# Kernel optimization log

Hardware: AMD Instinct MI355X
Metric: run time of the kernel (lower is better)

## Reference

```python
import jax, jax.numpy as jnp
import numpy as np

B, IN, EMB, HID, HYP, NZ = 8192, 512, 512, 1024, 256, 64
EPS = 1e-5


def _ln(x, g, b):
    # layernorm over last axis; g/b broadcast
    m = x.mean(-1, keepdims=True)
    v = x.var(-1, keepdims=True)
    return (x - m) * jax.lax.rsqrt(v + EPS) * g + b


def setup_inputs() -> dict:
    key = jax.random.key(0)
    ks = jax.random.split(key, 16)
    s = lambda i, shape: jax.random.normal(ks[i], shape, jnp.float32) * 0.02
    return dict(
        x=jax.random.normal(ks[0], (B, IN), jnp.float32),
        e=jax.random.normal(ks[1], (B, EMB), jnp.float32),
        h=jax.random.normal(ks[2], (B, HID), jnp.float32),
        c=jax.random.normal(ks[3], (B, HID), jnp.float32),
        h_hat=jax.random.normal(ks[4], (B, HYP), jnp.float32),
        c_hat=jax.random.normal(ks[5], (B, HYP), jnp.float32),
        # inner layer-normed LSTMCell(embedding_size, hyper_size) params
        hyper_Wx=s(6, (4 * HYP, EMB)),
        hyper_Wh=s(7, (4 * HYP, HYP)),
        hyper_b=jnp.zeros((4 * HYP,), jnp.float32),
        hyper_ln_g=jnp.ones((4, HYP), jnp.float32),
        hyper_ln_b=jnp.zeros((4, HYP), jnp.float32),
        hyper_lnc_g=jnp.ones((HYP,), jnp.float32),
        hyper_lnc_b=jnp.zeros((HYP,), jnp.float32),
        # z projections (hyper -> 4*n_z)
        zh_W=s(8, (4 * NZ, HYP)), zh_b=jnp.zeros((4 * NZ,), jnp.float32),
        zx_W=s(9, (4 * NZ, HYP)), zx_b=jnp.zeros((4 * NZ,), jnp.float32),
        zb_W=s(10, (4 * NZ, HYP)),
        # per-gate d projections (n_z -> hidden), no bias
        dh_W=s(11, (4, HID, NZ)),
        dx_W=s(12, (4, HID, NZ)),
        # outer LSTM weight matrices (zeros in torch init; randn here so outputs are nontrivial)
        w_h=s(13, (4, HID, HID)),
        w_x=s(14, (4, HID, IN)),
    )


def reference(x, e, h, c, h_hat, c_hat,
              hyper_Wx, hyper_Wh, hyper_b, hyper_ln_g, hyper_ln_b,
              hyper_lnc_g, hyper_lnc_b,
              zh_W, zh_b, zx_W, zx_b, zb_W, dh_W, dx_W, w_h, w_x):
    # --- inner layer-normed hyper LSTM cell ---
    ifgo = e @ hyper_Wx.T + h_hat @ hyper_Wh.T + hyper_b            # [B, 4*HYP]
    ifgo = _ln(ifgo.reshape(B, 4, HYP), hyper_ln_g, hyper_ln_b)     # per-gate LN
    i_g, f_g, g_g, o_g = (ifgo[:, k] for k in range(4))
    c_hat_n = jax.nn.sigmoid(f_g) * c_hat + jax.nn.sigmoid(i_g) * jnp.tanh(g_g)
    h_hat_n = jax.nn.sigmoid(o_g) * jnp.tanh(_ln(c_hat_n, hyper_lnc_g, hyper_lnc_b))
    # --- z vectors, chunked into 4 gates along last dim ---
    z_h = (h_hat_n @ zh_W.T + zh_b).reshape(B, 4, NZ)
    z_x = (h_hat_n @ zx_W.T + zx_b).reshape(B, 4, NZ)
    z_b = (h_hat_n @ zb_W.T).reshape(B, 4, NZ)
    # --- per-gate weight modulation: d = Linear(z); dhw = d @ W ---
    d_h = jnp.einsum('bgz,ghz->gbh', z_h, dh_W)        # [4, B, HID]
    d_x = jnp.einsum('bgz,ghz->gbh', z_x, dx_W)        # [4, B, HID]
    dhw_h = jnp.einsum('gbh,ghk->gbk', d_h, w_h)       # [4, B, HID]
    dhw_x = jnp.einsum('gbh,ghk->gbk', d_x, w_x)       # [4, B, IN]
    return dhw_h, dhw_x, jnp.transpose(z_b, (1, 0, 2))  # z_b chunks as [4, B, NZ]
```

## Files before the change

### kernel.cpp

```cpp
#include <hip/hip_runtime.h>
#include <cstddef>

constexpr int Bn   = 8192;
constexpr int INn  = 512;
constexpr int EMBn = 512;
constexpr int HIDn = 1024;
constexpr int HYPn = 256;
constexpr int NZn  = 64;
constexpr float EPS = 1e-5f;

typedef unsigned short u16;
typedef unsigned int   u32;
typedef float f32x4 __attribute__((ext_vector_type(4)));
typedef short s16x8 __attribute__((ext_vector_type(8)));

__device__ __forceinline__ u16 f2bf(float x) {
    u32 u = __float_as_uint(x);
    u = (u + 0x7FFFu + ((u >> 16) & 1u)) >> 16;
    return (u16)u;
}
__device__ __forceinline__ float bf2f(u16 h) {
    return __uint_as_float(((u32)h) << 16);
}

__global__ __launch_bounds__(256) void k_prep(
    const float* __restrict__ e,  const float* __restrict__ hh,
    const float* __restrict__ wx, const float* __restrict__ wh,
    u16* __restrict__ eHi, u16* __restrict__ eLo,
    u16* __restrict__ hhHi, u16* __restrict__ hhLo,
    u16* __restrict__ wxHi, u16* __restrict__ wxLo,
    u16* __restrict__ whHi, u16* __restrict__ whLo)
{
    long u = (long)blockIdx.x * 256 + threadIdx.x;
    const long U_E  = (long)Bn * EMBn / 8;
    const long U_H  = (long)Bn * HYPn / 8;
    const long U_WX = (long)HIDn * EMBn / 8;
    const float* src; u16 *hi, *lo; int ld, kblks;
    if (u < U_E)                    { src = e;  hi = eHi;  lo = eLo;  ld = EMBn; kblks = EMBn / 32; }
    else if (u < U_E + U_H)         { u -= U_E; src = hh; hi = hhHi; lo = hhLo; ld = HYPn; kblks = HYPn / 32; }
    else if (u < U_E + U_H + U_WX)  { u -= U_E + U_H; src = wx; hi = wxHi; lo = wxLo; ld = EMBn; kblks = EMBn / 32; }
    else                            { u -= U_E + U_H + U_WX; src = wh; hi = whHi; lo = whLo; ld = HYPn; kblks = HYPn / 32; }

    const long lu = u;
    const long perBlk = (long)kblks * 512;
    const int blk  = (int)(u / perBlk);
    const int rem  = (int)(u % perBlk);
    const int kblk = rem >> 9;
    const int r2   = rem & 511;
    const int grp  = r2 >> 6;
    const int lane = r2 & 63;
    const int row  = blk * 128 + grp * 16 + (lane & 15);
    const int k    = kblk * 32 + (lane >> 4) * 8;

    const float4 v0 = *(const float4*)(src + (size_t)row * ld + k);
    const float4 v1 = *(const float4*)(src + (size_t)row * ld + k + 4);
    const float f[8] = {v0.x, v0.y, v0.z, v0.w, v1.x, v1.y, v1.z, v1.w};
    union { u16 us[8]; uint4 v; } H, L;
#pragma unroll
    for (int j = 0; j < 8; ++j) {
        const u16 h = f2bf(f[j]);
        H.us[j] = h;
        L.us[j] = f2bf(f[j] - bf2f(h));
    }
    *(uint4*)(hi + lu * 8) = H.v;
    *(uint4*)(lo + lu * 8) = L.v;
}

__global__ __launch_bounds__(256) void k_ifgo_mfma(
    const u16* __restrict__ eHi,  const u16* __restrict__ eLo,
    const u16* __restrict__ hhHi, const u16* __restrict__ hhLo,
    const u16* __restrict__ wxHi, const u16* __restrict__ wxLo,
    const u16* __restrict__ whHi, const u16* __restrict__ whLo,
    const float* __restrict__ bias, float* __restrict__ ifgo)
{
    __shared__ __align__(16) u16 lds[4 * 4096];
    const int t = threadIdx.x;
    const int w = t >> 6, l = t & 63;
    const int wr = w >> 1, wc = w & 1;
    const int bx = blockIdx.x, by = blockIdx.y;

    f32x4 acc[4][4] = {};

    for (int s = 0; s < 24; ++s) {
        const bool seg0 = s < 16;
        const u16* aH = seg0 ? eHi  : hhHi;
        const u16* aL = seg0 ? eLo  : hhLo;
        const u16* bH = seg0 ? wxHi : whHi;
        const u16* bL = seg0 ? wxLo : whLo;
        const int kblks = seg0 ? 16 : 8;
        const int kb    = seg0 ? s : s - 16;
        const long ca = ((long)bx * kblks + kb) * 512;
        const long cb = ((long)by * kblks + kb) * 512;

        __syncthreads();
#pragma unroll
        for (int i = 0; i < 2; ++i) {
            const int un = i * 256 + t;
            __builtin_amdgcn_global_load_lds(
                (const __attribute__((address_space(1))) u32*)(aH + (ca + un) * 8),
                (__attribute__((address_space(3))) u32*)(lds + 0 * 4096 + un * 8), 16, 0, 0);
            __builtin_amdgcn_global_load_lds(
                (const __attribute__((address_space(1))) u32*)(aL + (ca + un) * 8),
                (__attribute__((address_space(3))) u32*)(lds + 1 * 4096 + un * 8), 16, 0, 0);
            __builtin_amdgcn_global_load_lds(
                (const __attribute__((address_space(1))) u32*)(bH + (cb + un) * 8),
                (__attribute__((address_space(3))) u32*)(lds + 2 * 4096 + un * 8), 16, 0, 0);
            __builtin_amdgcn_global_load_lds(
                (const __attribute__((address_space(1))) u32*)(bL + (cb + un) * 8),
                (__attribute__((address_space(3))) u32*)(lds + 3 * 4096 + un * 8), 16, 0, 0);
        }
        __syncthreads();

        s16x8 ah[4], al[4], bh[4], bl[4];
#pragma unroll
        for (int f = 0; f < 4; ++f) {
            const int ua = ((wr * 4 + f) * 64 + l) * 8;
            const int ub = ((wc * 4 + f) * 64 + l) * 8;
            ah[f] = *(const s16x8*)(lds + 0 * 4096 + ua);
            al[f] = *(const s16x8*)(lds + 1 * 4096 + ua);
            bh[f] = *(const s16x8*)(lds + 2 * 4096 + ub);
            bl[f] = *(const s16x8*)(lds + 3 * 4096 + ub);
        }
#pragma unroll
        for (int fm = 0; fm < 4; ++fm)
#pragma unroll
            for (int fn = 0; fn < 4; ++fn) {
                acc[fm][fn] = __builtin_amdgcn_mfma_f32_16x16x32_bf16(ah[fm], bh[fn], acc[fm][fn], 0, 0, 0);
                acc[fm][fn] = __builtin_amdgcn_mfma_f32_16x16x32_bf16(ah[fm], bl[fn], acc[fm][fn], 0, 0, 0);
                acc[fm][fn] = __builtin_amdgcn_mfma_f32_16x16x32_bf16(al[fm], bh[fn], acc[fm][fn], 0, 0, 0);
            }
    }

    const int row0 = bx * 128 + wr * 64;
    const int col0 = by * 128 + wc * 64;
    float bv[4];
#pragma unroll
    for (int fn = 0; fn < 4; ++fn) bv[fn] = bias[col0 + fn * 16 + (l & 15)];
#pragma unroll
    for (int fm = 0; fm < 4; ++fm) {
        const int r0 = row0 + fm * 16 + (l >> 4) * 4;
#pragma unroll
        for (int fn = 0; fn < 4; ++fn) {
            const int c = col0 + fn * 16 + (l & 15);
#pragma unroll
            for (int r = 0; r < 4; ++r)
                ifgo[(size_t)(r0 + r) * (4 * HYPn) + c] = acc[fm][fn][r] + bv[fn];
        }
    }
}

__device__ __forceinline__ void nt_accum(
    const float* __restrict__ A, const float* __restrict__ Bm,
    int K, int lda, int ldb, int row0, int col0, int t,
    float acc[4][4], float* As, float* Bs)
{
    const int lr = t >> 2;
    const int lk = (t & 3) << 2;
    const int ty = t >> 4;
    const int tx = t & 15;
    for (int k0 = 0; k0 < K; k0 += 16) {
        const float4 av = *(const float4*)(A  + (size_t)(row0 + lr) * lda + k0 + lk);
        const float4 bv = *(const float4*)(Bm + (size_t)(col0 + lr) * ldb + k0 + lk);
        __syncthreads();
        As[(lk + 0) * 68 + lr] = av.x; As[(lk + 1) * 68 + lr] = av.y;
        As[(lk + 2) * 68 + lr] = av.z; As[(lk + 3) * 68 + lr] = av.w;
        Bs[(lk + 0) * 68 + lr] = bv.x; Bs[(lk + 1) * 68 + lr] = bv.y;
        Bs[(lk + 2) * 68 + lr] = bv.z; Bs[(lk + 3) * 68 + lr] = bv.w;
        __syncthreads();
#pragma unroll
        for (int kk = 0; kk < 16; ++kk) {
            const float4 a = *(const float4*)(As + kk * 68 + ty * 4);
            const float4 b = *(const float4*)(Bs + kk * 68 + tx * 4);
            const float ar[4] = {a.x, a.y, a.z, a.w};
            const float br[4] = {b.x, b.y, b.z, b.w};
#pragma unroll
            for (int i = 0; i < 4; ++i)
#pragma unroll
                for (int j = 0; j < 4; ++j)
                    acc[i][j] = fmaf(ar[i], br[j], acc[i][j]);
        }
    }
}

__global__ __launch_bounds__(256) void k_cell(
    const float* __restrict__ ifgo, const float* __restrict__ c_hat,
    const float* __restrict__ ln_g, const float* __restrict__ ln_b,
    const float* __restrict__ lnc_g, const float* __restrict__ lnc_b,
    float* __restrict__ h_hat_n)
{
    const int row = blockIdx.x;
    const int t = threadIdx.x;
    const int lane = t & 63;
    const int wid = t >> 6;

    __shared__ float act[4][256];
    __shared__ float red[8];

    const float4 v = *(const float4*)(ifgo + (size_t)row * 1024 + t * 4);
    float s  = v.x + v.y + v.z + v.w;
    float ss = v.x * v.x + v.y * v.y + v.z * v.z + v.w * v.w;
#pragma unroll
    for (int off = 32; off > 0; off >>= 1) {
        s  += __shfl_xor(s, off);
        ss += __shfl_xor(ss, off);
    }
    const float m    = s * (1.f / 256.f);
    const float var  = fmaxf(ss * (1.f / 256.f) - m * m, 0.f);
    const float rstd = rsqrtf(var + EPS);

    const int jb = lane * 4;
    const float4 g4 = *(const float4*)(ln_g + wid * 256 + jb);
    const float4 b4 = *(const float4*)(ln_b + wid * 256 + jb);
    float y[4];
    y[0] = (v.x - m) * rstd * g4.x + b4.x;
    y[1] = (v.y - m) * rstd * g4.y + b4.y;
    y[2] = (v.z - m) * rstd * g4.z + b4.z;
    y[3] = (v.w - m) * rstd * g4.w + b4.w;
#pragma unroll
    for (int k = 0; k < 4; ++k) {
        float a;
        if (wid == 2) a = tanhf(y[k]);
        else          a = 1.f / (1.f + expf(-y[k]));
        act[wid][jb + k] = a;
    }
    __syncthreads();

    const float si = act[0][t];
    const float sf = act[1][t];
    const float tg = act[2][t];
    const float so = act[3][t];
    const float cn = sf * c_hat[(size_t)row * 256 + t] + si * tg;

    float s2 = cn, ss2 = cn * cn;
#pragma unroll
    for (int off = 32; off > 0; off >>= 1) {
        s2  += __shfl_xor(s2, off);
        ss2 += __shfl_xor(ss2, off);
    }
    if (lane == 0) { red[wid] = s2; red[4 + wid] = ss2; }
    __syncthreads();
    const float tot  = red[0] + red[1] + red[2] + red[3];
    const float tots = red[4] + red[5] + red[6] + red[7];
    const float m2   = tot * (1.f / 256.f);
    const float var2 = fmaxf(tots * (1.f / 256.f) - m2 * m2, 0.f);
    const float r2   = rsqrtf(var2 + EPS);
    const float hn   = so * tanhf((cn - m2) * r2 * lnc_g[t] + lnc_b[t]);
    h_hat_n[(size_t)row * 256 + t] = hn;
}

__global__ __launch_bounds__(256) void k_z_all(
    const float* __restrict__ hn,
    const float* __restrict__ zh_W, const float* __restrict__ zh_b,
    const float* __restrict__ zx_W, const float* __restrict__ zx_b,
    const float* __restrict__ zb_W,
    float* __restrict__ z_h, float* __restrict__ z_x, float* __restrict__ out3)
{
    __shared__ float As[16 * 68];
    __shared__ float Bs[16 * 68];
    float acc[4][4] = {};
    const int row0 = blockIdx.x * 64;
    const int seg  = blockIdx.y >> 2;
    const int col0 = (blockIdx.y & 3) * 64;
    const int t = threadIdx.x;

    const float* W = seg == 0 ? zh_W : (seg == 1 ? zx_W : zb_W);
    nt_accum(hn, W, HYPn, HYPn, HYPn, row0, col0, t, acc, As, Bs);

    const int ty = t >> 4, tx = t & 15;
    if (seg < 2) {
        const float* bias = seg == 0 ? zh_b : zx_b;
        float* out = seg == 0 ? z_h : z_x;
        const float4 bv = *(const float4*)(bias + col0 + tx * 4);
#pragma unroll
        for (int i = 0; i < 4; ++i) {
            float4 o;
            o.x = acc[i][0] + bv.x; o.y = acc[i][1] + bv.y;
            o.z = acc[i][2] + bv.z; o.w = acc[i][3] + bv.w;
            *(float4*)(out + (size_t)(row0 + ty * 4 + i) * 256 + col0 + tx * 4) = o;
        }
    } else {
        const int g = blockIdx.y & 3;
#pragma unroll
        for (int i = 0; i < 4; ++i) {
            float4 o;
            o.x = acc[i][0]; o.y = acc[i][1]; o.z = acc[i][2]; o.w = acc[i][3];
            *(float4*)(out3 + ((size_t)g * Bn + row0 + ty * 4 + i) * 64 + tx * 4) = o;
        }
    }
}

__global__ __launch_bounds__(256) void k_dm_part(
    const float* __restrict__ dh_W, const float* __restrict__ w_h,
    const float* __restrict__ dx_W, const float* __restrict__ w_x,
    float* __restrict__ pH, float* __restrict__ pX)
{
    const int tens = blockIdx.z >> 2;
    const int g    = blockIdx.z & 3;
    const int N    = tens ? INn : HIDn;
    if ((int)blockIdx.x * 64 >= N) return;
    const float* A  = (tens ? dx_W : dh_W) + (size_t)g * HIDn * NZn;
    const float* Bw = (tens ? w_x  : w_h ) + (size_t)g * HIDn * N;
    float* P = (tens ? pX : pH) + ((size_t)(g * 4 + blockIdx.y) * 64) * N;
    const int col0 = blockIdx.x * 64;
    const int hb   = blockIdx.y * 256;
    const int t = threadIdx.x;

    __shared__ float As[32 * 68];
    __shared__ float Bs[32 * 68];
    float acc[4][4] = {};
    const int lh = t >> 4;
    const int lc = (t & 15) * 4;
    const int ty = t >> 4, tx = t & 15;

    for (int h0 = hb; h0 < hb + 256; h0 += 32) {
        const float4 a0 = *(const float4*)(A  + (size_t)(h0 + lh)      * NZn + lc);
        const float4 a1 = *(const float4*)(A  + (size_t)(h0 + 16 + lh) * NZn + lc);
        const float4 b0 = *(const float4*)(Bw + (size_t)(h0 + lh)      * N + col0 + lc);
        const float4 b1 = *(const float4*)(Bw + (size_t)(h0 + 16 + lh) * N + col0 + lc);
        __syncthreads();
        *(float4*)(As + lh * 68 + lc)        = a0;
        *(float4*)(As + (16 + lh) * 68 + lc) = a1;
        *(float4*)(Bs + lh * 68 + lc)        = b0;
        *(float4*)(Bs + (16 + lh) * 68 + lc) = b1;
        __syncthreads();
#pragma unroll
        for (int kk = 0; kk < 32; ++kk) {
            const float4 a = *(const float4*)(As + kk * 68 + ty * 4);
            const float4 b = *(const float4*)(Bs + kk * 68 + tx * 4);
            const float ar[4] = {a.x, a.y, a.z, a.w};
            const float br[4] = {b.x, b.y, b.z, b.w};
#pragma unroll
            for (int i = 0; i < 4; ++i)
#pragma unroll
                for (int j = 0; j < 4; ++j)
                    acc[i][j] = fmaf(ar[i], br[j], acc[i][j]);
        }
    }
#pragma unroll
    for (int i = 0; i < 4; ++i) {
        float4 o;
        o.x = acc[i][0]; o.y = acc[i][1]; o.z = acc[i][2]; o.w = acc[i][3];
        *(float4*)(P + (size_t)(ty * 4 + i) * N + col0 + tx * 4) = o;
    }
}

__global__ __launch_bounds__(256) void k_red(
    const float* __restrict__ pH, const float* __restrict__ pX,
    float* __restrict__ M_h, float* __restrict__ M_x)
{
    const int NH4 = 4 * 64 * 1024 / 4;
    const int id = blockIdx.x * 256 + threadIdx.x;
    if (id < NH4) {
        const int per = 64 * 1024 / 4;
        const int g = id / per, r = id % per;
        const float4* b = (const float4*)pH + (size_t)g * 4 * per + r;
        const float4 a0 = b[0], a1 = b[per], a2 = b[2 * per], a3 = b[3 * per];
        float4 o;
        o.x = a0.x + a1.x + a2.x + a3.x; o.y = a0.y + a1.y + a2.y + a3.y;
        o.z = a0.z + a1.z + a2.z + a3.z; o.w = a0.w + a1.w + a2.w + a3.w;
        ((float4*)M_h)[id] = o;
    } else {
        const int id2 = id - NH4;
        const int per = 64 * 512 / 4;
        const int g = id2 / per, r = id2 % per;
        const float4* b = (const float4*)pX + (size_t)g * 4 * per + r;
        const float4 a0 = b[0], a1 = b[per], a2 = b[2 * per], a3 = b[3 * per];
        float4 o;
        o.x = a0.x + a1.x + a2.x + a3.x; o.y = a0.y + a1.y + a2.y + a3.y;
        o.z = a0.z + a1.z + a2.z + a3.z; o.w = a0.w + a1.w + a2.w + a3.w;
        ((float4*)M_x)[id2] = o;
    }
}

__global__ __launch_bounds__(256) void k_dhw(
    const float* __restrict__ Z, const float* __restrict__ M,
    float* __restrict__ out, int N)
{
    const int g = blockIdx.z;
    const float* A  = Z + g * NZn;
    const float* Bm = M + (size_t)g * NZn * N;
    float* C = out + (size_t)g * Bn * N;

    __shared__ float As[16 * 68];
    __shared__ float Bs[16 * 68];
    float acc[4][4] = {};
    const int row0 = blockIdx.x * 64;
    const int col0 = blockIdx.y * 64;
    const int t = threadIdx.x;
    const int lr = t >> 2;
    const int lk = (t & 3) << 2;
    const int bk = t >> 4;
    const int bc = (t & 15) * 4;
    const int ty = t >> 4, tx = t & 15;

    for (int k0 = 0; k0 < NZn; k0 += 16) {
        const float4 av = *(const float4*)(A  + (size_t)(row0 + lr) * HYPn + k0 + lk);
        const float4 bv = *(const float4*)(Bm + (size_t)(k0 + bk) * N + col0 + bc);
        __syncthreads();
        As[(lk + 0) * 68 + lr] = av.x; As[(lk + 1) * 68 + lr] = av.y;
        As[(lk + 2) * 68 + lr] = av.z; As[(lk + 3) * 68 + lr] = av.w;
        *(float4*)(Bs + bk * 68 + bc) = bv;
        __syncthreads();
#pragma unroll
        for (int kk = 0; kk < 16; ++kk) {
            const float4 a = *(const float4*)(As + kk * 68 + ty * 4);
            const float4 b = *(const float4*)(Bs + kk * 68 + tx * 4);
            const float ar[4] = {a.x, a.y, a.z, a.w};
            const float br[4] = {b.x, b.y, b.z, b.w};
#pragma unroll
            for (int i = 0; i < 4; ++i)
#pragma unroll
                for (int j = 0; j < 4; ++j)
                    acc[i][j] = fmaf(ar[i], br[j], acc[i][j]);
        }
    }
#pragma unroll
    for (int i = 0; i < 4; ++i) {
        float4 o;
        o.x = acc[i][0]; o.y = acc[i][1]; o.z = acc[i][2]; o.w = acc[i][3];
        *(float4*)(C + (size_t)(row0 + ty * 4 + i) * N + col0 + tx * 4) = o;
    }
}

extern "C" void kernel_launch(void* const* d_in, const int* in_sizes, int n_in,
                              void* d_out, int out_size, void* d_ws, size_t ws_size,
                              hipStream_t stream)
{
    const float* e        = (const float*)d_in[1];
    const float* h_hat    = (const float*)d_in[4];
    const float* c_hat    = (const float*)d_in[5];
    const float* hyper_Wx = (const float*)d_in[6];
    const float* hyper_Wh = (const float*)d_in[7];
    const float* hyper_b  = (const float*)d_in[8];
    const float* ln_g     = (const float*)d_in[9];
    const float* ln_b     = (const float*)d_in[10];
    const float* lnc_g    = (const float*)d_in[11];
    const float* lnc_b    = (const float*)d_in[12];
    const float* zh_W     = (const float*)d_in[13];
    const float* zh_b     = (const float*)d_in[14];
    const float* zx_W     = (const float*)d_in[15];
    const float* zx_b     = (const float*)d_in[16];
    const float* zb_W     = (const float*)d_in[17];
    const float* dh_W     = (const float*)d_in[18];
    const float* dx_W     = (const float*)d_in[19];
    const float* w_h      = (const float*)d_in[20];
    const float* w_x      = (const float*)d_in[21];

    float* out1 = (float*)d_out;
    float* out2 = out1 + (size_t)4 * Bn * HIDn;
    float* out3 = out2 + (size_t)4 * Bn * INn;

    float* ws   = (float*)d_ws;
    float* ifgo = ws;  ws += (size_t)Bn * 1024;
    float* hn   = ws;  ws += (size_t)Bn * HYPn;
    float* z_h  = ws;  ws += (size_t)Bn * HYPn;
    float* z_x  = ws;  ws += (size_t)Bn * HYPn;
    float* M_h  = ws;  ws += (size_t)4 * NZn * HIDn;
    float* M_x  = ws;  ws += (size_t)4 * NZn * INn;
    float* pH   = ws;  ws += (size_t)16 * NZn * HIDn;
    float* pX   = ws;  ws += (size_t)16 * NZn * INn;
    u16* bp   = (u16*)ws;
    u16* eHi  = bp;  bp += (size_t)Bn * EMBn;
    u16* eLo  = bp;  bp += (size_t)Bn * EMBn;
    u16* hhHi = bp;  bp += (size_t)Bn * HYPn;
    u16* hhLo = bp;  bp += (size_t)Bn * HYPn;
    u16* wxHi = bp;  bp += (size_t)HIDn * EMBn;
    u16* wxLo = bp;  bp += (size_t)HIDn * EMBn;
    u16* whHi = bp;  bp += (size_t)HIDn * HYPn;
    u16* whLo = bp;  bp += (size_t)HIDn * HYPn;

    k_prep<<<dim3(3456), 256, 0, stream>>>(e, h_hat, hyper_Wx, hyper_Wh,
        eHi, eLo, hhHi, hhLo, wxHi, wxLo, whHi, whLo);
    k_dm_part<<<dim3(16, 4, 8), 256, 0, stream>>>(dh_W, w_h, dx_W, w_x, pH, pX);
    k_red<<<dim3(384), 256, 0, stream>>>(pH, pX, M_h, M_x);
    k_ifgo_mfma<<<dim3(64, 8), 256, 0, stream>>>(
        eHi, eLo, hhHi, hhLo, wxHi, wxLo, whHi, whLo, hyper_b, ifgo);
    k_cell<<<dim3(Bn), 256, 0, stream>>>(ifgo, c_hat, ln_g, ln_b, lnc_g, lnc_b, hn);
    k_z_all<<<dim3(Bn / 64, 12), 256, 0, stream>>>(
        hn, zh_W, zh_b, zx_W, zx_b, zb_W, z_h, z_x, out3);
    k_dhw<<<dim3(Bn / 64, HIDn / 64, 4), 256, 0, stream>>>(z_h, M_h, out1, HIDn);
    k_dhw<<<dim3(Bn / 64, INn / 64, 4), 256, 0, stream>>>(z_x, M_x, out2, INn);
}
```

Measured before the change: 512.4 us.

## Fold z projections into the weight products and run one split-bf16 MFMA output GEMM

Precomputes P = zW^T·M per gate in a new kernel, so each output becomes hn @ P + W_b·M. This replaces the scalar-FMA z projection and the two K=64 dhw GEMMs with a single K=256 three-term split-bf16 MFMA GEMM that writes out1, out2 and out3 directly. The cost removed is the fp32 FMA GEMMs and the z_h/z_x intermediates. In exchange there are more FLOPs (K=256 instead of 64), an extra hn conversion pass, scattered scalar stores in the epilogue, and a small change in rounding behaviour.

```diff
diff --git a/kernel.cpp b/kernel.cpp
--- a/kernel.cpp
+++ b/kernel.cpp
@@ -26,20 +26,24 @@
 __global__ __launch_bounds__(256) void k_prep(
     const float* __restrict__ e,  const float* __restrict__ hh,
     const float* __restrict__ wx, const float* __restrict__ wh,
+    const float* __restrict__ zb,
     u16* __restrict__ eHi, u16* __restrict__ eLo,
     u16* __restrict__ hhHi, u16* __restrict__ hhLo,
     u16* __restrict__ wxHi, u16* __restrict__ wxLo,
-    u16* __restrict__ whHi, u16* __restrict__ whLo)
+    u16* __restrict__ whHi, u16* __restrict__ whLo,
+    u16* __restrict__ zbHi, u16* __restrict__ zbLo)
 {
     long u = (long)blockIdx.x * 256 + threadIdx.x;
     const long U_E  = (long)Bn * EMBn / 8;
     const long U_H  = (long)Bn * HYPn / 8;
     const long U_WX = (long)HIDn * EMBn / 8;
+    const long U_WH = (long)HIDn * HYPn / 8;
     const float* src; u16 *hi, *lo; int ld, kblks;
-    if (u < U_E)                    { src = e;  hi = eHi;  lo = eLo;  ld = EMBn; kblks = EMBn / 32; }
-    else if (u < U_E + U_H)         { u -= U_E; src = hh; hi = hhHi; lo = hhLo; ld = HYPn; kblks = HYPn / 32; }
-    else if (u < U_E + U_H + U_WX)  { u -= U_E + U_H; src = wx; hi = wxHi; lo = wxLo; ld = EMBn; kblks = EMBn / 32; }
-    else                            { u -= U_E + U_H + U_WX; src = wh; hi = whHi; lo = whLo; ld = HYPn; kblks = HYPn / 32; }
+    if (u < U_E)                          { src = e;  hi = eHi;  lo = eLo;  ld = EMBn; kblks = EMBn / 32; }
+    else if (u < U_E + U_H)               { u -= U_E; src = hh; hi = hhHi; lo = hhLo; ld = HYPn; kblks = HYPn / 32; }
+    else if (u < U_E + U_H + U_WX)        { u -= U_E + U_H; src = wx; hi = wxHi; lo = wxLo; ld = EMBn; kblks = EMBn / 32; }
+    else if (u < U_E + U_H + U_WX + U_WH) { u -= U_E + U_H + U_WX; src = wh; hi = whHi; lo = whLo; ld = HYPn; kblks = HYPn / 32; }
+    else                                  { u -= U_E + U_H + U_WX + U_WH; src = zb; hi = zbHi; lo = zbLo; ld = HYPn; kblks = HYPn / 32; }
 
     const long lu = u;
     const long perBlk = (long)kblks * 512;
@@ -66,6 +70,32 @@
     *(uint4*)(lo + lu * 8) = L.v;
 }
 
+__global__ __launch_bounds__(256) void k_prep1(
+    const float* __restrict__ src, u16* __restrict__ hi, u16* __restrict__ lo)
+{
+    const long u = (long)blockIdx.x * 256 + threadIdx.x;
+    const int blk  = (int)(u >> 12);
+    const int rem  = (int)(u & 4095);
+    const int kblk = rem >> 9;
+    const int r2   = rem & 511;
+    const int lane = r2 & 63;
+    const int row  = blk * 128 + (r2 >> 6) * 16 + (lane & 15);
+    const int k    = kblk * 32 + (lane >> 4) * 8;
+
+    const float4 v0 = *(const float4*)(src + (size_t)row * HYPn + k);
+    const float4 v1 = *(const float4*)(src + (size_t)row * HYPn + k + 4);
+    const float f[8] = {v0.x, v0.y, v0.z, v0.w, v1.x, v1.y, v1.z, v1.w};
+    union { u16 us[8]; uint4 v; } H, L;
+#pragma unroll
+    for (int j = 0; j < 8; ++j) {
+        const u16 h = f2bf(f[j]);
+        H.us[j] = h;
+        L.us[j] = f2bf(f[j] - bf2f(h));
+    }
+    *(uint4*)(hi + u * 8) = H.v;
+    *(uint4*)(lo + u * 8) = L.v;
+}
+
 __global__ __launch_bounds__(256) void k_ifgo_mfma(
     const u16* __restrict__ eHi,  const u16* __restrict__ eLo,
     const u16* __restrict__ hhHi, const u16* __restrict__ hhLo,
@@ -149,39 +179,6 @@
     }
 }
 
-__device__ __forceinline__ void nt_accum(
-    const float* __restrict__ A, const float* __restrict__ Bm,
-    int K, int lda, int ldb, int row0, int col0, int t,
-    float acc[4][4], float* As, float* Bs)
-{
-    const int lr = t >> 2;
-    const int lk = (t & 3) << 2;
-    const int ty = t >> 4;
-    const int tx = t & 15;
-    for (int k0 = 0; k0 < K; k0 += 16) {
-        const float4 av = *(const float4*)(A  + (size_t)(row0 + lr) * lda + k0 + lk);
-        const float4 bv = *(const float4*)(Bm + (size_t)(col0 + lr) * ldb + k0 + lk);
-        __syncthreads();
-        As[(lk + 0) * 68 + lr] = av.x; As[(lk + 1) * 68 + lr] = av.y;
-        As[(lk + 2) * 68 + lr] = av.z; As[(lk + 3) * 68 + lr] = av.w;
-        Bs[(lk + 0) * 68 + lr] = bv.x; Bs[(lk + 1) * 68 + lr] = bv.y;
-        Bs[(lk + 2) * 68 + lr] = bv.z; Bs[(lk + 3) * 68 + lr] = bv.w;
-        __syncthreads();
-#pragma unroll
-        for (int kk = 0; kk < 16; ++kk) {
-            const float4 a = *(const float4*)(As + kk * 68 + ty * 4);
-            const float4 b = *(const float4*)(Bs + kk * 68 + tx * 4);
-            const float ar[4] = {a.x, a.y, a.z, a.w};
-            const float br[4] = {b.x, b.y, b.z, b.w};
-#pragma unroll
-            for (int i = 0; i < 4; ++i)
-#pragma unroll
-                for (int j = 0; j < 4; ++j)
-                    acc[i][j] = fmaf(ar[i], br[j], acc[i][j]);
-        }
-    }
-}
-
 __global__ __launch_bounds__(256) void k_cell(
     const float* __restrict__ ifgo, const float* __restrict__ c_hat,
     const float* __restrict__ ln_g, const float* __restrict__ ln_b,
@@ -246,47 +243,6 @@
     const float r2   = rsqrtf(var2 + EPS);
     const float hn   = so * tanhf((cn - m2) * r2 * lnc_g[t] + lnc_b[t]);
     h_hat_n[(size_t)row * 256 + t] = hn;
-}
-
-__global__ __launch_bounds__(256) void k_z_all(
-    const float* __restrict__ hn,
-    const float* __restrict__ zh_W, const float* __restrict__ zh_b,
-    const float* __restrict__ zx_W, const float* __restrict__ zx_b,
-    const float* __restrict__ zb_W,
-    float* __restrict__ z_h, float* __restrict__ z_x, float* __restrict__ out3)
-{
-    __shared__ float As[16 * 68];
-    __shared__ float Bs[16 * 68];
-    float acc[4][4] = {};
-    const int row0 = blockIdx.x * 64;
-    const int seg  = blockIdx.y >> 2;
-    const int col0 = (blockIdx.y & 3) * 64;
-    const int t = threadIdx.x;
-
-    const float* W = seg == 0 ? zh_W : (seg == 1 ? zx_W : zb_W);
-    nt_accum(hn, W, HYPn, HYPn, HYPn, row0, col0, t, acc, As, Bs);
-
-    const int ty = t >> 4, tx = t & 15;
-    if (seg < 2) {
-        const float* bias = seg == 0 ? zh_b : zx_b;
-        float* out = seg == 0 ? z_h : z_x;
-        const float4 bv = *(const float4*)(bias + col0 + tx * 4);
-#pragma unroll
-        for (int i = 0; i < 4; ++i) {
-            float4 o;
-            o.x = acc[i][0] + bv.x; o.y = acc[i][1] + bv.y;
-            o.z = acc[i][2] + bv.z; o.w = acc[i][3] + bv.w;
-            *(float4*)(out + (size_t)(row0 + ty * 4 + i) * 256 + col0 + tx * 4) = o;
-        }
-    } else {
-        const int g = blockIdx.y & 3;
-#pragma unroll
-        for (int i = 0; i < 4; ++i) {
-            float4 o;
-            o.x = acc[i][0]; o.y = acc[i][1]; o.z = acc[i][2]; o.w = acc[i][3];
-            *(float4*)(out3 + ((size_t)g * Bn + row0 + ty * 4 + i) * 64 + tx * 4) = o;
-        }
-    }
 }
 
 __global__ __launch_bounds__(256) void k_dm_part(
@@ -372,53 +328,173 @@
     }
 }
 
-__global__ __launch_bounds__(256) void k_dhw(
-    const float* __restrict__ Z, const float* __restrict__ M,
-    float* __restrict__ out, int N)
-{
-    const int g = blockIdx.z;
-    const float* A  = Z + g * NZn;
-    const float* Bm = M + (size_t)g * NZn * N;
-    float* C = out + (size_t)g * Bn * N;
-
-    __shared__ float As[16 * 68];
-    __shared__ float Bs[16 * 68];
-    float acc[4][4] = {};
-    const int row0 = blockIdx.x * 64;
-    const int col0 = blockIdx.y * 64;
+__global__ __launch_bounds__(256) void k_p2(
+    const float* __restrict__ zh_W, const float* __restrict__ zh_b,
+    const float* __restrict__ zx_W, const float* __restrict__ zx_b,
+    const float* __restrict__ M_h,  const float* __restrict__ M_x,
+    u16* __restrict__ phHi, u16* __restrict__ phLo,
+    u16* __restrict__ pxHi, u16* __restrict__ pxLo,
+    float* __restrict__ cbias)
+{
+    const int cb  = blockIdx.x;
+    const int ks4 = blockIdx.y;
+    const bool isH = cb < 32;
+    const int g    = isH ? (cb >> 3) : ((cb - 32) >> 2);
+    const int N    = isH ? HIDn : INn;
+    const int cloc = isH ? ((cb & 7) * 128) : (((cb - 32) & 3) * 128);
+    const float* W  = (isH ? zh_W : zx_W) + (size_t)g * 64 * HYPn;
+    const float* bb = (isH ? zh_b : zx_b) + g * 64;
+    const float* M  = (isH ? M_h  : M_x ) + (size_t)g * 64 * N + cloc;
+    u16* pHi = isH ? phHi : pxHi;
+    u16* pLo = isH ? phLo : pxLo;
+    const long ubase = (long)(isH ? cb : cb - 32) * 4096;
     const int t = threadIdx.x;
-    const int lr = t >> 2;
-    const int lk = (t & 3) << 2;
-    const int bk = t >> 4;
-    const int bc = (t & 15) * 4;
-    const int ty = t >> 4, tx = t & 15;
-
-    for (int k0 = 0; k0 < NZn; k0 += 16) {
-        const float4 av = *(const float4*)(A  + (size_t)(row0 + lr) * HYPn + k0 + lk);
-        const float4 bv = *(const float4*)(Bm + (size_t)(k0 + bk) * N + col0 + bc);
+
+    __shared__ float Ms[128 * 65];
+    __shared__ float Wsh[64 * 64];
+    for (int i = t; i < 8192; i += 256) {
+        const int z = i >> 7, c = i & 127;
+        Ms[c * 65 + z] = M[(size_t)z * N + c];
+    }
+    for (int i = t; i < 4096; i += 256) {
+        const int z = i >> 6, kk = i & 63;
+        Wsh[z * 64 + kk] = W[(size_t)z * 256 + ks4 * 64 + kk];
+    }
+    __syncthreads();
+
+    for (int uu = t; uu < 1024; uu += 256) {
+        const int kbl  = uu >> 9;
+        const int r2   = uu & 511;
+        const int lane = r2 & 63;
+        const int c    = (r2 >> 6) * 16 + (lane & 15);
+        const int kloc = kbl * 32 + (lane >> 4) * 8;
+        float p0 = 0.f, p1 = 0.f, p2 = 0.f, p3 = 0.f;
+        float p4 = 0.f, p5 = 0.f, p6 = 0.f, p7 = 0.f;
+#pragma unroll 8
+        for (int z = 0; z < 64; ++z) {
+            const float m = Ms[c * 65 + z];
+            const float4 w0 = *(const float4*)(Wsh + z * 64 + kloc);
+            const float4 w1 = *(const float4*)(Wsh + z * 64 + kloc + 4);
+            p0 = fmaf(w0.x, m, p0); p1 = fmaf(w0.y, m, p1);
+            p2 = fmaf(w0.z, m, p2); p3 = fmaf(w0.w, m, p3);
+            p4 = fmaf(w1.x, m, p4); p5 = fmaf(w1.y, m, p5);
+            p6 = fmaf(w1.z, m, p6); p7 = fmaf(w1.w, m, p7);
+        }
+        const float pv[8] = {p0, p1, p2, p3, p4, p5, p6, p7};
+        union { u16 us[8]; uint4 v; } H, L;
+#pragma unroll
+        for (int j = 0; j < 8; ++j) {
+            const u16 h = f2bf(pv[j]);
+            H.us[j] = h;
+            L.us[j] = f2bf(pv[j] - bf2f(h));
+        }
+        const long uo = ubase + (long)(ks4 * 2 + kbl) * 512 + r2;
+        *(uint4*)(pHi + uo * 8) = H.v;
+        *(uint4*)(pLo + uo * 8) = L.v;
+    }
+    if (ks4 == 0 && t < 128) {
+        float a = 0.f;
+#pragma unroll 8
+        for (int z = 0; z < 64; ++z) a = fmaf(bb[z], Ms[t * 65 + z], a);
+        cbias[cb * 128 + t] = a;
+    }
+}
+
+__global__ __launch_bounds__(256) void k_out(
+    const u16* __restrict__ hnHi, const u16* __restrict__ hnLo,
+    const u16* __restrict__ phHi, const u16* __restrict__ phLo,
+    const u16* __restrict__ pxHi, const u16* __restrict__ pxLo,
+    const u16* __restrict__ zbHi, const u16* __restrict__ zbLo,
+    const float* __restrict__ cbias,
+    float* __restrict__ out1, float* __restrict__ out2, float* __restrict__ out3)
+{
+    __shared__ __align__(16) u16 lds[4 * 4096];
+    const int t = threadIdx.x;
+    const int w = t >> 6, l = t & 63;
+    const int wr = w >> 1, wc = w & 1;
+    const int bx = blockIdx.x, by = blockIdx.y;
+
+    const u16 *bH, *bL; long cbB;
+    if (by < 32)      { bH = phHi; bL = phLo; cbB = (long)by * 4096; }
+    else if (by < 48) { bH = pxHi; bL = pxLo; cbB = (long)(by - 32) * 4096; }
+    else              { bH = zbHi; bL = zbLo; cbB = (long)(by - 48) * 4096; }
+    const long caB = (long)bx * 4096;
+
+    f32x4 acc[4][4] = {};
+
+    for (int s = 0; s < 8; ++s) {
+        const long ca = caB + (long)s * 512;
+        const long cb = cbB + (long)s * 512;
         __syncthreads();
-        As[(lk + 0) * 68 + lr] = av.x; As[(lk + 1) * 68 + lr] = av.y;
-        As[(lk + 2) * 68 + lr] = av.z; As[(lk + 3) * 68 + lr] = av.w;
-        *(float4*)(Bs + bk * 68 + bc) = bv;
+#pragma unroll
+        for (int i = 0; i < 2; ++i) {
+            const int un = i * 256 + t;
+            __builtin_amdgcn_global_load_lds(
+                (const __attribute__((address_space(1))) u32*)(hnHi + (ca + un) * 8),
+                (__attribute__((address_space(3))) u32*)(lds + 0 * 4096 + un * 8), 16, 0, 0);
+            __builtin_amdgcn_global_load_lds(
+                (const __attribute__((address_space(1))) u32*)(hnLo + (ca + un) * 8),
+                (__attribute__((address_space(3))) u32*)(lds + 1 * 4096 + un * 8), 16, 0, 0);
+            __builtin_amdgcn_global_load_lds(
+                (const __attribute__((address_space(1))) u32*)(bH + (cb + un) * 8),
+                (__attribute__((address_space(3))) u32*)(lds + 2 * 4096 + un * 8), 16, 0, 0);
+            __builtin_amdgcn_global_load_lds(
+                (const __attribute__((address_space(1))) u32*)(bL + (cb + un) * 8),
+                (__attribute__((address_space(3))) u32*)(lds + 3 * 4096 + un * 8), 16, 0, 0);
+        }
         __syncthreads();
-#pragma unroll
-        for (int kk = 0; kk < 16; ++kk) {
-            const float4 a = *(const float4*)(As + kk * 68 + ty * 4);
-            const float4 b = *(const float4*)(Bs + kk * 68 + tx * 4);
-            const float ar[4] = {a.x, a.y, a.z, a.w};
-            const float br[4] = {b.x, b.y, b.z, b.w};
-#pragma unroll
-            for (int i = 0; i < 4; ++i)
-#pragma unroll
-                for (int j = 0; j < 4; ++j)
-                    acc[i][j] = fmaf(ar[i], br[j], acc[i][j]);
-        }
-    }
-#pragma unroll
-    for (int i = 0; i < 4; ++i) {
-        float4 o;
-        o.x = acc[i][0]; o.y = acc[i][1]; o.z = acc[i][2]; o.w = acc[i][3];
-        *(float4*)(C + (size_t)(row0 + ty * 4 + i) * N + col0 + tx * 4) = o;
+
+        s16x8 ah[4], al[4], bh[4], bl[4];
+#pragma unroll
+        for (int f = 0; f < 4; ++f) {
+            const int ua = ((wr * 4 + f) * 64 + l) * 8;
+            const int ub = ((wc * 4 + f) * 64 + l) * 8;
+            ah[f] = *(const s16x8*)(lds + 0 * 4096 + ua);
+            al[f] = *(const s16x8*)(lds + 1 * 4096 + ua);
+            bh[f] = *(const s16x8*)(lds + 2 * 4096 + ub);
+            bl[f] = *(const s16x8*)(lds + 3 * 4096 + ub);
+        }
+#pragma unroll
+        for (int fm = 0; fm < 4; ++fm)
+#pragma unroll
+            for (int fn = 0; fn < 4; ++fn) {
+                acc[fm][fn] = __builtin_amdgcn_mfma_f32_16x16x32_bf16(ah[fm], bh[fn], acc[fm][fn], 0, 0, 0);
+                acc[fm][fn] = __builtin_amdgcn_mfma_f32_16x16x32_bf16(ah[fm], bl[fn], acc[fm][fn], 0, 0, 0);
+                acc[fm][fn] = __builtin_amdgcn_mfma_f32_16x16x32_bf16(al[fm], bh[fn], acc[fm][fn], 0, 0, 0);
+            }
+    }
+
+    const int row0 = bx * 128 + wr * 64;
+    const int colb = by * 128 + wc * 64;
+#pragma unroll
+    for (int fn = 0; fn < 4; ++fn) {
+        const int col = colb + fn * 16 + (l & 15);
+        float bias; float* base; int ld2;
+        if (col < 4096) {
+            bias = cbias[col];
+            const int g = col >> 10;
+            base = out1 + (size_t)g * Bn * 1024 + (col & 1023);
+            ld2 = 1024;
+        } else if (col < 6144) {
+            bias = cbias[col];
+            const int cg = col - 4096;
+            const int g = cg >> 9;
+            base = out2 + (size_t)g * Bn * 512 + (cg & 511);
+            ld2 = 512;
+        } else {
+            bias = 0.f;
+            const int cg = col - 6144;
+            const int g = cg >> 6;
+            base = out3 + (size_t)g * Bn * 64 + (cg & 63);
+            ld2 = 64;
+        }
+#pragma unroll
+        for (int fm = 0; fm < 4; ++fm) {
+            const int r0 = row0 + fm * 16 + (l >> 4) * 4;
+#pragma unroll
+            for (int r = 0; r < 4; ++r)
+                base[(size_t)(r0 + r) * ld2] = acc[fm][fn][r] + bias;
+        }
     }
 }
 
@@ -450,34 +526,42 @@
     float* out2 = out1 + (size_t)4 * Bn * HIDn;
     float* out3 = out2 + (size_t)4 * Bn * INn;
 
-    float* ws   = (float*)d_ws;
-    float* ifgo = ws;  ws += (size_t)Bn * 1024;
-    float* hn   = ws;  ws += (size_t)Bn * HYPn;
-    float* z_h  = ws;  ws += (size_t)Bn * HYPn;
-    float* z_x  = ws;  ws += (size_t)Bn * HYPn;
-    float* M_h  = ws;  ws += (size_t)4 * NZn * HIDn;
-    float* M_x  = ws;  ws += (size_t)4 * NZn * INn;
-    float* pH   = ws;  ws += (size_t)16 * NZn * HIDn;
-    float* pX   = ws;  ws += (size_t)16 * NZn * INn;
-    u16* bp   = (u16*)ws;
-    u16* eHi  = bp;  bp += (size_t)Bn * EMBn;
-    u16* eLo  = bp;  bp += (size_t)Bn * EMBn;
-    u16* hhHi = bp;  bp += (size_t)Bn * HYPn;
-    u16* hhLo = bp;  bp += (size_t)Bn * HYPn;
-    u16* wxHi = bp;  bp += (size_t)HIDn * EMBn;
-    u16* wxLo = bp;  bp += (size_t)HIDn * EMBn;
-    u16* whHi = bp;  bp += (size_t)HIDn * HYPn;
-    u16* whLo = bp;  bp += (size_t)HIDn * HYPn;
-
-    k_prep<<<dim3(3456), 256, 0, stream>>>(e, h_hat, hyper_Wx, hyper_Wh,
-        eHi, eLo, hhHi, hhLo, wxHi, wxLo, whHi, whLo);
+    float* ws    = (float*)d_ws;
+    float* ifgo  = ws;  ws += (size_t)Bn * 1024;
+    float* hn    = ws;  ws += (size_t)Bn * HYPn;
+    float* M_h   = ws;  ws += (size_t)4 * NZn * HIDn;
+    float* M_x   = ws;  ws += (size_t)4 * NZn * INn;
+    float* pH    = ws;  ws += (size_t)16 * NZn * HIDn;
+    float* pX    = ws;  ws += (size_t)16 * NZn * INn;
+    float* cbias = ws;  ws += 6144;
+    u16* bp    = (u16*)ws;
+    u16* eHi   = bp;  bp += (size_t)Bn * EMBn;
+    u16* eLo   = bp;  bp += (size_t)Bn * EMBn;
+    u16* hhHi  = bp;  bp += (size_t)Bn * HYPn;
+    u16* hhLo  = bp;  bp += (size_t)Bn * HYPn;
+    u16* wxHi  = bp;  bp += (size_t)HIDn * EMBn;
+    u16* wxLo  = bp;  bp += (size_t)HIDn * EMBn;
+    u16* whHi  = bp;  bp += (size_t)HIDn * HYPn;
+    u16* whLo  = bp;  bp += (size_t)HIDn * HYPn;
+    u16* zbHi  = bp;  bp += (size_t)HYPn * HYPn;
+    u16* zbLo  = bp;  bp += (size_t)HYPn * HYPn;
+    u16* hnHi  = bp;  bp += (size_t)Bn * HYPn;
+    u16* hnLo  = bp;  bp += (size_t)Bn * HYPn;
+    u16* phHi  = bp;  bp += (size_t)4096 * HYPn;
+    u16* phLo  = bp;  bp += (size_t)4096 * HYPn;
+    u16* pxHi  = bp;  bp += (size_t)2048 * HYPn;
+    u16* pxLo  = bp;
+
+    k_prep<<<dim3(3488), 256, 0, stream>>>(e, h_hat, hyper_Wx, hyper_Wh, zb_W,
+        eHi, eLo, hhHi, hhLo, wxHi, wxLo, whHi, whLo, zbHi, zbLo);
     k_dm_part<<<dim3(16, 4, 8), 256, 0, stream>>>(dh_W, w_h, dx_W, w_x, pH, pX);
     k_red<<<dim3(384), 256, 0, stream>>>(pH, pX, M_h, M_x);
+    k_p2<<<dim3(48, 4), 256, 0, stream>>>(zh_W, zh_b, zx_W, zx_b, M_h, M_x,
+        phHi, phLo, pxHi, pxLo, cbias);
     k_ifgo_mfma<<<dim3(64, 8), 256, 0, stream>>>(
         eHi, eLo, hhHi, hhLo, wxHi, wxLo, whHi, whLo, hyper_b, ifgo);
     k_cell<<<dim3(Bn), 256, 0, stream>>>(ifgo, c_hat, ln_g, ln_b, lnc_g, lnc_b, hn);
-    k_z_all<<<dim3(Bn / 64, 12), 256, 0, stream>>>(
-        hn, zh_W, zh_b, zx_W, zx_b, zb_W, z_h, z_x, out3);
-    k_dhw<<<dim3(Bn / 64, HIDn / 64, 4), 256, 0, stream>>>(z_h, M_h, out1, HIDn);
-    k_dhw<<<dim3(Bn / 64, INn / 64, 4), 256, 0, stream>>>(z_x, M_x, out2, INn);
-}
+    k_prep1<<<dim3(1024), 256, 0, stream>>>(hn, hnHi, hnLo);
+    k_out<<<dim3(64, 50), 256, 0, stream>>>(hnHi, hnLo, phHi, phLo, pxHi, pxLo,
+        zbHi, zbLo, cbias, out1, out2, out3);
+}
```

Measured after the change: 495.2 us. 3.4% less time.
